# Kernel tuning notes

Measured on AMD Instinct MI355X. Metric: run time of the kernel, lower is better.

The kernel has to match this reference:

```python
import jax, jax.numpy as jnp
import numpy as np

B, T, C, H = 2, 2048, 1024, 16
HS = C // H  # head_size = 64
EPS = 1e-5


def setup_inputs() -> dict:
    key = jax.random.key(0)
    ks = jax.random.split(key, 12)
    s = 0.02
    return {
        "x": jax.random.normal(ks[0], (B, T, C), jnp.float32),
        # per-head q/k/v linears stacked on a leading head axis [H, C, HS]
        "Wq": jax.random.normal(ks[1], (H, C, HS), jnp.float32) * s,
        "bq": jnp.zeros((H, HS), jnp.float32),
        "Wk": jax.random.normal(ks[2], (H, C, HS), jnp.float32) * s,
        "bk": jnp.zeros((H, HS), jnp.float32),
        "Wv": jax.random.normal(ks[3], (H, C, HS), jnp.float32) * s,
        "bv": jnp.zeros((H, HS), jnp.float32),
        # output projection [H*HS, C] == [C, C]
        "Wo": jax.random.normal(ks[4], (C, C), jnp.float32) * s,
        "bo": jnp.zeros((C,), jnp.float32),
        # feed-forward: C -> 4C -> C
        "W1": jax.random.normal(ks[5], (C, 4 * C), jnp.float32) * s,
        "b1": jnp.zeros((4 * C,), jnp.float32),
        "W2": jax.random.normal(ks[6], (4 * C, C), jnp.float32) * s,
        "b2": jnp.zeros((C,), jnp.float32),
        # custom LayerNorm params (broadcast over last dim)
        "gamma1": jnp.ones((C,), jnp.float32),
        "beta1": jnp.zeros((C,), jnp.float32),
        "gamma2": jnp.ones((C,), jnp.float32),
        "beta2": jnp.zeros((C,), jnp.float32),
    }


def _ln(x, gamma, beta):
    # NOTE: faithful to the source: normalizes over axis=1 (the SEQUENCE axis
    # for [B,T,C] input), uses unbiased variance (torch default), and puts eps
    # OUTSIDE the sqrt: (x - mean) / (sqrt(var) + eps).
    mean = x.mean(axis=1, keepdims=True)
    var = x.var(axis=1, keepdims=True, ddof=1)
    return gamma * ((x - mean) / (jnp.sqrt(var) + EPS)) + beta


def reference(x, Wq, bq, Wk, bk, Wv, bv, Wo, bo, W1, b1, W2, b2,
              gamma1, beta1, gamma2, beta2):
    # --- self-attention sublayer (pre-norm, residual) ---
    h = _ln(x, gamma1, beta1)
    q = jnp.einsum('btc,hcd->bhtd', h, Wq) + bq[None, :, None, :]
    k = jnp.einsum('btc,hcd->bhtd', h, Wk) + bk[None, :, None, :]
    v = jnp.einsum('btc,hcd->bhtd', h, Wv) + bv[None, :, None, :]
    wei = jax.nn.softmax(jnp.einsum('bhtd,bhsd->bhts', q, k) * (HS ** -0.5), axis=-1)
    attn = jnp.einsum('bhts,bhsd->bhtd', wei, v)          # [B,H,T,HS]
    attn = attn.transpose(0, 2, 1, 3).reshape(B, T, H * HS)  # head-order concat
    x = x + attn @ Wo + bo
    # --- feed-forward sublayer (pre-norm, residual) ---
    h2 = _ln(x, gamma2, beta2)
    x = x + jax.nn.relu(h2 @ W1 + b1) @ W2 + b2
    return x
```

## Files before the change

kernel.cpp:

```cpp
#include <hip/hip_runtime.h>
#include <hip/hip_bf16.h>

#define Bq 2
#define Tq 2048
#define Cq 1024
#define Hq 16
#define HSq 64
#define EPSq 1e-5f

using bf16 = __hip_bfloat16;
using f32x4 = __attribute__((ext_vector_type(4))) float;
using f32x16 = __attribute__((ext_vector_type(16))) float;
using bf16x8 = __attribute__((ext_vector_type(8))) __bf16;

__device__ __forceinline__ bf16 f2bf(float f) { return __float2bfloat16(f); }
__device__ __forceinline__ unsigned short f2u(float f) {
    return __builtin_bit_cast(unsigned short, __float2bfloat16(f));
}
__device__ __forceinline__ void gload16(const void* g, void* l) {
    __builtin_amdgcn_global_load_lds((const __attribute__((address_space(1))) void*)g,
                                     (__attribute__((address_space(3))) void*)l, 16, 0, 0);
}

__global__ void k_transpose(const float* __restrict__ src, bf16* __restrict__ dst,
                            int R, int Cc, long strideSrc, long strideDst) {
    __shared__ bf16 tile[32][33];
    const long zb = blockIdx.z;
    src += zb * strideSrc;
    dst += zb * strideDst;
    int c0 = blockIdx.x * 32, r0 = blockIdx.y * 32;
    int tx = threadIdx.x & 31, ty = threadIdx.x >> 5;
    for (int i = ty; i < 32; i += 8)
        tile[i][tx] = f2bf(src[(long)(r0 + i) * Cc + (c0 + tx)]);
    __syncthreads();
    for (int i = ty; i < 32; i += 8)
        dst[(long)(c0 + i) * R + (r0 + tx)] = tile[tx][i];
}

__global__ void k_pack_bias(const float* __restrict__ a, const float* __restrict__ b,
                            const float* __restrict__ c, float* __restrict__ dst) {
    int i = blockIdx.x * 256 + threadIdx.x;
    dst[i] = a[i];
    dst[1024 + i] = b[i];
    dst[2048 + i] = c[i];
}

__global__ void k_ln_part(const float* __restrict__ x, float* __restrict__ ps,
                          float* __restrict__ pss) {
    int c = blockIdx.x * 256 + threadIdx.x;
    int b = blockIdx.y;
    int tc = blockIdx.z;
    const float* p = x + (long)b * Tq * Cq + (long)tc * 64 * Cq + c;
    float s = 0.f, ss = 0.f;
    for (int t = 0; t < 64; ++t) {
        float v = p[(long)t * Cq];
        s += v;
        ss += v * v;
    }
    long o = ((long)tc * Bq + b) * Cq + c;
    ps[o] = s;
    pss[o] = ss;
}

__global__ void k_ln_fin(const float* __restrict__ ps, const float* __restrict__ pss,
                         float* __restrict__ mean, float* __restrict__ rstd) {
    int i = blockIdx.x * 256 + threadIdx.x;
    float s = 0.f, ss = 0.f;
    for (int tc = 0; tc < 32; ++tc) {
        s += ps[(long)tc * (Bq * Cq) + i];
        ss += pss[(long)tc * (Bq * Cq) + i];
    }
    float m = s / (float)Tq;
    float var = (ss - s * m) / (float)(Tq - 1);
    var = fmaxf(var, 0.f);
    mean[i] = m;
    rstd[i] = 1.0f / (sqrtf(var) + EPSq);
}

__global__ void k_ln_apply(const float* __restrict__ x, const float* __restrict__ mean,
                           const float* __restrict__ rstd, const float* __restrict__ gamma,
                           const float* __restrict__ beta, bf16* __restrict__ out) {
    long i = (long)blockIdx.x * 256 + threadIdx.x;
    int c = (int)(i & (Cq - 1));
    long bt = i >> 10;
    int b = (int)(bt >> 11);
    float m = mean[b * Cq + c], r = rstd[b * Cq + c];
    out[i] = f2bf(gamma[c] * ((x[i] - m) * r) + beta[c]);
}

template <int MODE>
__global__ __launch_bounds__(256, 3) void k_gemm_nt(
    const bf16* __restrict__ A, int lda, const bf16* __restrict__ Bt, int ldb, int K,
    const float* __restrict__ bias, bf16* __restrict__ outB, int ldout) {
    __shared__ __bf16 sA[2][128 * 32];
    __shared__ __bf16 sB[2][128 * 32];
    const int m0 = blockIdx.y * 128, n0 = blockIdx.x * 128;
    const int tid = threadIdx.x;
    const int lane = tid & 63, wave = tid >> 6;
    const int lane15 = lane & 15, quad = lane >> 4;
    const int wm = (wave >> 1) * 64, wn = (wave & 1) * 64;
    const int srow = wave * 16 + (lane >> 2);
    const int scol = (lane & 3) * 8;
    __bf16* a00 = &sA[0][wave * 512];
    __bf16* a01 = &sA[0][2048 + wave * 512];
    __bf16* a10 = &sA[1][wave * 512];
    __bf16* a11 = &sA[1][2048 + wave * 512];
    __bf16* b00 = &sB[0][wave * 512];
    __bf16* b01 = &sB[0][2048 + wave * 512];
    __bf16* b10 = &sB[1][wave * 512];
    __bf16* b11 = &sB[1][2048 + wave * 512];
    const bf16* Ap = A + (long)(m0 + srow) * lda + scol;
    const bf16* Ap2 = Ap + 64L * lda;
    const bf16* Bp = Bt + (long)(n0 + srow) * ldb + scol;
    const bf16* Bp2 = Bp + 64L * ldb;

    f32x4 acc[4][4];
#pragma unroll
    for (int i = 0; i < 4; ++i)
#pragma unroll
        for (int j = 0; j < 4; ++j)
#pragma unroll
            for (int p = 0; p < 4; ++p) acc[i][j][p] = 0.f;

    for (int k0 = 0; k0 < K; k0 += 64) {
        __syncthreads();
        gload16(Ap + k0, a00);
        gload16(Ap2 + k0, a01);
        gload16(Ap + k0 + 32, a10);
        gload16(Ap2 + k0 + 32, a11);
        gload16(Bp + k0, b00);
        gload16(Bp2 + k0, b01);
        gload16(Bp + k0 + 32, b10);
        gload16(Bp2 + k0 + 32, b11);
        __syncthreads();
#pragma unroll
        for (int kk = 0; kk < 2; ++kk) {
            bf16x8 af[4], bfr[4];
#pragma unroll
            for (int i = 0; i < 4; ++i)
                af[i] = *(const bf16x8*)(&sA[kk][(wm + i * 16 + lane15) * 32 + quad * 8]);
#pragma unroll
            for (int j = 0; j < 4; ++j)
                bfr[j] = *(const bf16x8*)(&sB[kk][(wn + j * 16 + lane15) * 32 + quad * 8]);
#pragma unroll
            for (int i = 0; i < 4; ++i)
#pragma unroll
                for (int j = 0; j < 4; ++j)
                    acc[i][j] = __builtin_amdgcn_mfma_f32_16x16x32_bf16(af[i], bfr[j],
                                                                        acc[i][j], 0, 0, 0);
        }
    }
    if (MODE == 0) {
#pragma unroll
        for (int i = 0; i < 4; ++i) {
            const int mm = m0 + wm + i * 16 + quad * 4;
            const int b = mm >> 11, t4 = mm & (Tq - 1);
#pragma unroll
            for (int j = 0; j < 4; ++j) {
                const int n = n0 + wn + j * 16 + lane15;
                const int which = n >> 10, hh = (n >> 6) & (Hq - 1), d = n & (HSq - 1);
                const long bh = (long)b * Hq + hh;
                const float bb = bias[n];
                if (which == 0) {
#pragma unroll
                    for (int p = 0; p < 4; ++p)
                        outB[bh * 131072 + (long)(t4 + p) * HSq + d] =
                            f2bf((acc[i][j][p] + bb) * 0.125f);
                } else if (which == 1) {
#pragma unroll
                    for (int p = 0; p < 4; ++p)
                        outB[4194304L + bh * 131072 + (long)(t4 + p) * HSq + d] =
                            f2bf(acc[i][j][p] + bb);
                } else {
                    ushort4 pk;
                    pk.x = f2u(acc[i][j][0] + bb);
                    pk.y = f2u(acc[i][j][1] + bb);
                    pk.z = f2u(acc[i][j][2] + bb);
                    pk.w = f2u(acc[i][j][3] + bb);
                    *(ushort4*)(&outB[8388608L + bh * 131072 + (long)d * Tq + t4]) = pk;
                }
            }
        }
    } else {
#pragma unroll
        for (int i = 0; i < 4; ++i) {
#pragma unroll
            for (int p = 0; p < 4; ++p) {
                const int m = m0 + wm + i * 16 + quad * 4 + p;
#pragma unroll
                for (int j = 0; j < 4; ++j) {
                    const int n = n0 + wn + j * 16 + lane15;
                    outB[(long)m * ldout + n] = f2bf(fmaxf(acc[i][j][p] + bias[n], 0.f));
                }
            }
        }
    }
}

template <int MODE>
__global__ __launch_bounds__(256, 4) void k_gemm_n64(
    const bf16* __restrict__ A, int lda, const bf16* __restrict__ Bt, int ldb, int K,
    const float* __restrict__ bias, const float* __restrict__ residF,
    float* __restrict__ outF, int ldout) {
    __shared__ __bf16 sA[2][128 * 32];
    __shared__ __bf16 sB[2][64 * 32];
    const int m0 = blockIdx.y * 128, n0 = blockIdx.x * 64;
    const int tid = threadIdx.x;
    const int lane = tid & 63, wave = tid >> 6;
    const int lane15 = lane & 15, quad = lane >> 4;
    const int wm = wave * 32;
    const int srow = wave * 16 + (lane >> 2);
    const int scol = (lane & 3) * 8;
    __bf16* a00 = &sA[0][wave * 512];
    __bf16* a01 = &sA[0][2048 + wave * 512];
    __bf16* a10 = &sA[1][wave * 512];
    __bf16* a11 = &sA[1][2048 + wave * 512];
    __bf16* b00 = &sB[0][wave * 512];
    __bf16* b10 = &sB[1][wave * 512];
    const bf16* Ap = A + (long)(m0 + srow) * lda + scol;
    const bf16* Ap2 = Ap + 64L * lda;
    const bf16* Bp = Bt + (long)(n0 + srow) * ldb + scol;

    f32x4 acc[2][4];
#pragma unroll
    for (int i = 0; i < 2; ++i)
#pragma unroll
        for (int j = 0; j < 4; ++j)
#pragma unroll
            for (int p = 0; p < 4; ++p) acc[i][j][p] = 0.f;

    for (int k0 = 0; k0 < K; k0 += 64) {
        __syncthreads();
        gload16(Ap + k0, a00);
        gload16(Ap2 + k0, a01);
        gload16(Ap + k0 + 32, a10);
        gload16(Ap2 + k0 + 32, a11);
        gload16(Bp + k0, b00);
        gload16(Bp + k0 + 32, b10);
        __syncthreads();
#pragma unroll
        for (int kk = 0; kk < 2; ++kk) {
            bf16x8 af[2], bfr[4];
#pragma unroll
            for (int i = 0; i < 2; ++i)
                af[i] = *(const bf16x8*)(&sA[kk][(wm + i * 16 + lane15) * 32 + quad * 8]);
#pragma unroll
            for (int j = 0; j < 4; ++j)
                bfr[j] = *(const bf16x8*)(&sB[kk][(j * 16 + lane15) * 32 + quad * 8]);
#pragma unroll
            for (int i = 0; i < 2; ++i)
#pragma unroll
                for (int j = 0; j < 4; ++j)
                    acc[i][j] = __builtin_amdgcn_mfma_f32_16x16x32_bf16(af[i], bfr[j],
                                                                        acc[i][j], 0, 0, 0);
        }
    }
#pragma unroll
    for (int i = 0; i < 2; ++i) {
#pragma unroll
        for (int p = 0; p < 4; ++p) {
            const int m = m0 + wm + i * 16 + quad * 4 + p;
#pragma unroll
            for (int j = 0; j < 4; ++j) {
                const int n = n0 + j * 16 + lane15;
                outF[(long)m * ldout + n] =
                    acc[i][j][p] + bias[n] + residF[(long)m * ldout + n];
            }
        }
    }
}

__global__ __launch_bounds__(256, 2) void k_attn(const bf16* __restrict__ qkv,
                                                 bf16* __restrict__ attn) {
    __shared__ __bf16 sK[64 * 72];
    __shared__ __bf16 sVt[64 * 72];
    const int bh = blockIdx.y;
    const int q0 = blockIdx.x * 128;
    const int tid = threadIdx.x, wave = tid >> 6, lane = tid & 63;
    const int lane31 = lane & 31, laneh = lane >> 5;
    const bf16* Qp = qkv + (long)bh * 131072;
    const bf16* Kp = qkv + 4194304L + (long)bh * 131072;
    const bf16* Vtp = qkv + 8388608L + (long)bh * 131072;
    bf16x8 qa[4];
#pragma unroll
    for (int s = 0; s < 4; ++s)
        qa[s] = *(const bf16x8*)(&Qp[(long)(q0 + wave * 32 + lane31) * HSq + s * 16 + laneh * 8]);
    f32x16 o[2];
#pragma unroll
    for (int dt = 0; dt < 2; ++dt)
#pragma unroll
        for (int r = 0; r < 16; ++r) o[dt][r] = 0.f;
    float rs = 0.f;
    const int r0 = tid >> 3, c0 = (tid & 7) * 8;
    const int r1 = r0 + 32;

    uint4 nk0 = *(const uint4*)(&Kp[(long)r0 * HSq + c0]);
    uint4 nk1 = *(const uint4*)(&Kp[(long)r1 * HSq + c0]);
    uint4 nv0 = *(const uint4*)(&Vtp[(long)r0 * Tq + c0]);
    uint4 nv1 = *(const uint4*)(&Vtp[(long)r1 * Tq + c0]);

    for (int kc = 0; kc < Tq; kc += 64) {
        __syncthreads();
        *(uint4*)(&sK[r0 * 72 + c0]) = nk0;
        *(uint4*)(&sK[r1 * 72 + c0]) = nk1;
        *(uint4*)(&sVt[r0 * 72 + c0]) = nv0;
        *(uint4*)(&sVt[r1 * 72 + c0]) = nv1;
        __syncthreads();
        if (kc + 64 < Tq) {
            nk0 = *(const uint4*)(&Kp[(long)(kc + 64 + r0) * HSq + c0]);
            nk1 = *(const uint4*)(&Kp[(long)(kc + 64 + r1) * HSq + c0]);
            nv0 = *(const uint4*)(&Vtp[(long)r0 * Tq + kc + 64 + c0]);
            nv1 = *(const uint4*)(&Vtp[(long)r1 * Tq + kc + 64 + c0]);
        }
#pragma unroll
        for (int nt = 0; nt < 2; ++nt) {
            f32x16 z;
#pragma unroll
            for (int r = 0; r < 16; ++r) z[r] = 0.f;
#pragma unroll
            for (int s = 0; s < 4; ++s) {
                bf16x8 kb =
                    *(const bf16x8*)(&sK[(nt * 32 + lane31) * 72 + s * 16 + laneh * 8]);
                z = __builtin_amdgcn_mfma_f32_32x32x16_bf16(kb, qa[s], z, 0, 0, 0);
            }
            float e[16];
#pragma unroll
            for (int r = 0; r < 16; ++r) {
                e[r] = __expf(z[r]);
                rs += e[r];
            }
            unsigned int pk[8];
#pragma unroll
            for (int g = 0; g < 4; ++g)
#pragma unroll
                for (int h = 0; h < 2; ++h)
                    pk[g * 2 + h] = (unsigned int)f2u(e[g * 4 + 2 * h]) |
                                    ((unsigned int)f2u(e[g * 4 + 2 * h + 1]) << 16);
            unsigned int sa0 = laneh ? pk[0] : pk[2], sa1 = laneh ? pk[1] : pk[3];
            unsigned int ra0 = __shfl_xor((int)sa0, 32), ra1 = __shfl_xor((int)sa1, 32);
            unsigned int sb0 = laneh ? pk[4] : pk[6], sb1 = laneh ? pk[5] : pk[7];
            unsigned int rb0 = __shfl_xor((int)sb0, 32), rb1 = __shfl_xor((int)sb1, 32);
            uint4 f0, f1;
            if (laneh == 0) {
                f0 = {pk[0], pk[1], ra0, ra1};
                f1 = {pk[4], pk[5], rb0, rb1};
            } else {
                f0 = {ra0, ra1, pk[2], pk[3]};
                f1 = {rb0, rb1, pk[6], pk[7]};
            }
            bf16x8 pa0 = __builtin_bit_cast(bf16x8, f0);
            bf16x8 pa1 = __builtin_bit_cast(bf16x8, f1);
#pragma unroll
            for (int dt = 0; dt < 2; ++dt) {
                bf16x8 vb0 =
                    *(const bf16x8*)(&sVt[(dt * 32 + lane31) * 72 + nt * 32 + laneh * 8]);
                bf16x8 vb1 = *(const bf16x8*)(&sVt[(dt * 32 + lane31) * 72 + nt * 32 + 16 +
                                                   laneh * 8]);
                o[dt] = __builtin_amdgcn_mfma_f32_32x32x16_bf16(pa0, vb0, o[dt], 0, 0, 0);
                o[dt] = __builtin_amdgcn_mfma_f32_32x32x16_bf16(pa1, vb1, o[dt], 0, 0, 0);
            }
        }
    }
    float ltot = rs + __shfl_xor(rs, 32);
    float linv = 1.0f / ltot;
    const int b = bh >> 4, hh = bh & 15;
#pragma unroll
    for (int r = 0; r < 16; ++r) {
        const int tl = (r & 3) + 8 * (r >> 2) + 4 * laneh;
        float inv = __shfl(linv, tl);
        const int t = q0 + wave * 32 + tl;
        const long base = ((long)b * Tq + t) * Cq + hh * HSq;
#pragma unroll
        for (int dt = 0; dt < 2; ++dt)
            attn[base + dt * 32 + lane31] = f2bf(o[dt][r] * inv);
    }
}

extern "C" void kernel_launch(void* const* d_in, const int* in_sizes, int n_in,
                              void* d_out, int out_size, void* d_ws, size_t ws_size,
                              hipStream_t stream) {
    const float* x = (const float*)d_in[0];
    const float* Wq = (const float*)d_in[1];
    const float* bqv = (const float*)d_in[2];
    const float* Wk = (const float*)d_in[3];
    const float* bkv = (const float*)d_in[4];
    const float* Wv = (const float*)d_in[5];
    const float* bvv = (const float*)d_in[6];
    const float* Wo = (const float*)d_in[7];
    const float* bo = (const float*)d_in[8];
    const float* W1 = (const float*)d_in[9];
    const float* b1 = (const float*)d_in[10];
    const float* W2 = (const float*)d_in[11];
    const float* b2 = (const float*)d_in[12];
    const float* g1 = (const float*)d_in[13];
    const float* be1 = (const float*)d_in[14];
    const float* g2 = (const float*)d_in[15];
    const float* be2 = (const float*)d_in[16];

    char* ws = (char*)d_ws;
    size_t off = 0;
    auto alloc = [&](size_t bytes) {
        void* p = ws + off;
        off += (bytes + 255) & ~(size_t)255;
        return p;
    };
    bf16* regA = (bf16*)alloc(32L * 1024 * 1024);
    float* x2 = (float*)alloc(4096L * 1024 * 4);
    bf16* buf1 = (bf16*)alloc(4096L * 1024 * 2);
    float* bqkv = (float*)alloc(3072L * 4);
    float* ps = (float*)alloc(32L * Bq * Cq * 4);
    float* pss = (float*)alloc(32L * Bq * Cq * 4);
    float* mean1 = (float*)alloc(Bq * Cq * 4);
    float* rstd1 = (float*)alloc(Bq * Cq * 4);
    float* mean2 = (float*)alloc(Bq * Cq * 4);
    float* rstd2 = (float*)alloc(Bq * Cq * 4);
    bf16* dres = (bf16*)d_out;
    float* outF = (float*)d_out;

    k_ln_part<<<dim3(4, Bq, 32), 256, 0, stream>>>(x, ps, pss);
    k_ln_fin<<<dim3(8), 256, 0, stream>>>(ps, pss, mean1, rstd1);
    k_ln_apply<<<dim3(16384), 256, 0, stream>>>(x, mean1, rstd1, g1, be1, dres);

    k_transpose<<<dim3(2, 32, 16), 256, 0, stream>>>(Wq, buf1, 1024, 64, 65536, 65536);
    k_transpose<<<dim3(2, 32, 16), 256, 0, stream>>>(Wk, buf1 + 1048576, 1024, 64, 65536, 65536);
    k_transpose<<<dim3(2, 32, 16), 256, 0, stream>>>(Wv, buf1 + 2097152, 1024, 64, 65536, 65536);
    k_pack_bias<<<dim3(4), 256, 0, stream>>>(bqv, bkv, bvv, bqkv);
    k_gemm_nt<0><<<dim3(24, 32), 256, 0, stream>>>(dres, 1024, buf1, 1024, 1024, bqkv, regA, 0);
    k_attn<<<dim3(16, 32), 256, 0, stream>>>(regA, dres);
    k_transpose<<<dim3(32, 32, 1), 256, 0, stream>>>(Wo, buf1, 1024, 1024, 0, 0);
    k_gemm_n64<1><<<dim3(16, 32), 256, 0, stream>>>(dres, 1024, buf1, 1024, 1024, bo, x, x2,
                                                    1024);
    k_ln_part<<<dim3(4, Bq, 32), 256, 0, stream>>>(x2, ps, pss);
    k_ln_fin<<<dim3(8), 256, 0, stream>>>(ps, pss, mean2, rstd2);
    k_ln_apply<<<dim3(16384), 256, 0, stream>>>(x2, mean2, rstd2, g2, be2, dres);

    k_transpose<<<dim3(128, 32, 1), 256, 0, stream>>>(W1, buf1, 1024, 4096, 0, 0);
    k_gemm_nt<2><<<dim3(32, 32), 256, 0, stream>>>(dres, 1024, buf1, 1024, 1024, b1, regA, 4096);
    k_transpose<<<dim3(32, 128, 1), 256, 0, stream>>>(W2, buf1, 4096, 1024, 0, 0);
    k_gemm_n64<3><<<dim3(16, 32), 256, 0, stream>>>(regA, 4096, buf1, 4096, 4096, b2, x2, outF,
                                                    1024);
}
```

Measured before the change: 391.6 us.

## Swizzle GEMM LDS layout, remap blocks across XCDs, raise MFMA wave priority

Both GEMM kernels now use an XOR-swizzled column offset for the global-to-LDS copy and for the fragment reads, to reduce LDS bank conflicts. Block indices are remapped so consecutive tiles land on the same XCD, which should improve L2 reuse. The attention kernel wraps its MFMA sections in s_setprio so waves issuing matrix work are favoured over waves doing exp/shuffle work. The swizzle has to match exactly between the writes and the reads, and the XCD remap assumes the block count is divisible by 8.

```diff
diff --git a/kernel.cpp b/kernel.cpp
--- a/kernel.cpp
+++ b/kernel.cpp
@@ -88,19 +88,31 @@
     out[i] = f2bf(gamma[c] * ((x[i] - m) * r) + beta[c]);
 }
 
+__device__ __forceinline__ void xcd_swizzle(int& bx, int& by) {
+    const int gx = gridDim.x;
+    const int nwg = gx * gridDim.y;
+    const int bid = blockIdx.y * gx + blockIdx.x;
+    const int swz = (bid & 7) * (nwg >> 3) + (bid >> 3);
+    bx = swz % gx;
+    by = swz / gx;
+}
+
 template <int MODE>
 __global__ __launch_bounds__(256, 3) void k_gemm_nt(
     const bf16* __restrict__ A, int lda, const bf16* __restrict__ Bt, int ldb, int K,
     const float* __restrict__ bias, bf16* __restrict__ outB, int ldout) {
     __shared__ __bf16 sA[2][128 * 32];
     __shared__ __bf16 sB[2][128 * 32];
-    const int m0 = blockIdx.y * 128, n0 = blockIdx.x * 128;
+    int bx, by;
+    xcd_swizzle(bx, by);
+    const int m0 = by * 128, n0 = bx * 128;
     const int tid = threadIdx.x;
     const int lane = tid & 63, wave = tid >> 6;
     const int lane15 = lane & 15, quad = lane >> 4;
     const int wm = (wave >> 1) * 64, wn = (wave & 1) * 64;
     const int srow = wave * 16 + (lane >> 2);
-    const int scol = (lane & 3) * 8;
+    const int scol = (((lane & 3) ^ ((lane >> 3) & 3)) * 8);
+    const int sq8 = (quad ^ ((lane15 >> 1) & 3)) * 8;
     __bf16* a00 = &sA[0][wave * 512];
     __bf16* a01 = &sA[0][2048 + wave * 512];
     __bf16* a10 = &sA[1][wave * 512];
@@ -138,10 +150,10 @@
             bf16x8 af[4], bfr[4];
 #pragma unroll
             for (int i = 0; i < 4; ++i)
-                af[i] = *(const bf16x8*)(&sA[kk][(wm + i * 16 + lane15) * 32 + quad * 8]);
+                af[i] = *(const bf16x8*)(&sA[kk][(wm + i * 16 + lane15) * 32 + sq8]);
 #pragma unroll
             for (int j = 0; j < 4; ++j)
-                bfr[j] = *(const bf16x8*)(&sB[kk][(wn + j * 16 + lane15) * 32 + quad * 8]);
+                bfr[j] = *(const bf16x8*)(&sB[kk][(wn + j * 16 + lane15) * 32 + sq8]);
 #pragma unroll
             for (int i = 0; i < 4; ++i)
 #pragma unroll
@@ -204,13 +216,16 @@
     float* __restrict__ outF, int ldout) {
     __shared__ __bf16 sA[2][128 * 32];
     __shared__ __bf16 sB[2][64 * 32];
-    const int m0 = blockIdx.y * 128, n0 = blockIdx.x * 64;
+    int bx, by;
+    xcd_swizzle(bx, by);
+    const int m0 = by * 128, n0 = bx * 64;
     const int tid = threadIdx.x;
     const int lane = tid & 63, wave = tid >> 6;
     const int lane15 = lane & 15, quad = lane >> 4;
     const int wm = wave * 32;
     const int srow = wave * 16 + (lane >> 2);
-    const int scol = (lane & 3) * 8;
+    const int scol = (((lane & 3) ^ ((lane >> 3) & 3)) * 8);
+    const int sq8 = (quad ^ ((lane15 >> 1) & 3)) * 8;
     __bf16* a00 = &sA[0][wave * 512];
     __bf16* a01 = &sA[0][2048 + wave * 512];
     __bf16* a10 = &sA[1][wave * 512];
@@ -243,10 +258,10 @@
             bf16x8 af[2], bfr[4];
 #pragma unroll
             for (int i = 0; i < 2; ++i)
-                af[i] = *(const bf16x8*)(&sA[kk][(wm + i * 16 + lane15) * 32 + quad * 8]);
+                af[i] = *(const bf16x8*)(&sA[kk][(wm + i * 16 + lane15) * 32 + sq8]);
 #pragma unroll
             for (int j = 0; j < 4; ++j)
-                bfr[j] = *(const bf16x8*)(&sB[kk][(j * 16 + lane15) * 32 + quad * 8]);
+                bfr[j] = *(const bf16x8*)(&sB[kk][(j * 16 + lane15) * 32 + sq8]);
 #pragma unroll
             for (int i = 0; i < 2; ++i)
 #pragma unroll
@@ -317,12 +332,14 @@
             f32x16 z;
 #pragma unroll
             for (int r = 0; r < 16; ++r) z[r] = 0.f;
+            __builtin_amdgcn_s_setprio(1);
 #pragma unroll
             for (int s = 0; s < 4; ++s) {
                 bf16x8 kb =
                     *(const bf16x8*)(&sK[(nt * 32 + lane31) * 72 + s * 16 + laneh * 8]);
                 z = __builtin_amdgcn_mfma_f32_32x32x16_bf16(kb, qa[s], z, 0, 0, 0);
             }
+            __builtin_amdgcn_s_setprio(0);
             float e[16];
 #pragma unroll
             for (int r = 0; r < 16; ++r) {
@@ -350,6 +367,7 @@
             }
             bf16x8 pa0 = __builtin_bit_cast(bf16x8, f0);
             bf16x8 pa1 = __builtin_bit_cast(bf16x8, f1);
+            __builtin_amdgcn_s_setprio(1);
 #pragma unroll
             for (int dt = 0; dt < 2; ++dt) {
                 bf16x8 vb0 =
@@ -359,6 +377,7 @@
                 o[dt] = __builtin_amdgcn_mfma_f32_32x32x16_bf16(pa0, vb0, o[dt], 0, 0, 0);
                 o[dt] = __builtin_amdgcn_mfma_f32_32x32x16_bf16(pa1, vb1, o[dt], 0, 0, 0);
             }
+            __builtin_amdgcn_s_setprio(0);
         }
     }
     float ltot = rs + __shfl_xor(rs, 32);
```

Result: no change. 392.6 us (+0.3%).
